# Performance work log

Hardware: AMD Instinct MI355X
Metric: run time of the kernel (lower is better)

## Reference

```python
import jax, jax.numpy as jnp
import numpy as np

N = 8192
HIDDEN = 1024
PROJ = 128
T = 0.07
LN_EPS = 1e-12


def _neg_indices(n):
    # Static [n, n-2] index matrix: for row i, all j except j==i and the
    # paired sample j == (i + n//2) % n. Computed with numpy (n is static).
    half = n // 2
    idx = np.arange(n)
    mask = np.ones((n, n), dtype=bool)
    mask[idx, idx] = False
    mask[idx, (idx + half) % n] = False
    return np.nonzero(mask)[1].reshape(n, n - 2)


def setup_inputs() -> dict:
    key = jax.random.key(0)
    ks = jax.random.split(key, 3)
    scale = 1.0 / np.sqrt(HIDDEN)
    return {
        "x": jax.random.normal(ks[0], (N, HIDDEN), dtype=jnp.float32),
        "dense_w": jax.random.normal(ks[1], (HIDDEN, HIDDEN), dtype=jnp.float32) * scale,
        "dense_b": jnp.zeros((HIDDEN,), dtype=jnp.float32),
        "ln_gamma": jnp.ones((HIDDEN,), dtype=jnp.float32),
        "ln_beta": jnp.zeros((HIDDEN,), dtype=jnp.float32),
        "dec_w": jax.random.normal(ks[2], (HIDDEN, PROJ), dtype=jnp.float32) * scale,
        "dec_b": jnp.zeros((PROJ,), dtype=jnp.float32),
    }


def reference(x, dense_w, dense_b, ln_gamma, ln_beta, dec_w, dec_b):
    # dense -> gelu (exact, erf-based as in BERT) -> layernorm -> decoder
    h = x @ dense_w + dense_b
    h = jax.nn.gelu(h, approximate=False)
    mu = jnp.mean(h, axis=-1, keepdims=True)
    var = jnp.mean(jnp.square(h - mu), axis=-1, keepdims=True)
    h = (h - mu) * jax.lax.rsqrt(var + LN_EPS) * ln_gamma + ln_beta
    z = h @ dec_w + dec_b  # [N, 128]

    n = z.shape[0]
    half = n // 2
    # positive logit: dot(z_i, z_partner)
    l_pos = jnp.sum(z[:half] * z[half:], axis=-1)  # [N/2]
    l_pos = jnp.concatenate([l_pos, l_pos])[:, None]  # [N, 1]

    # full similarity matrix, then gather the N-2 negatives per row
    sims = z @ z.T  # [N, N]
    neg_idx = jnp.asarray(_neg_indices(n))  # static [N, N-2]
    l_neg = jnp.take_along_axis(sims, neg_idx, axis=1)  # [N, N-2]

    logits = jnp.concatenate([l_pos, l_neg], axis=1) / T  # [N, N-1]
    # CrossEntropyLoss with labels == 0
    loss = jnp.mean(jax.nn.logsumexp(logits, axis=-1) - logits[:, 0])
    return loss
```

## Files before the change

kernel.cpp:

```cpp
#include <hip/hip_runtime.h>
#include <math.h>
#include <stdint.h>

#define NN 8192
#define HID 1024
#define PROJ 128

constexpr float INV_T = 1.0f / 0.07f;
constexpr float LN_EPS = 1e-12f;
constexpr float CC = 14.285714285714286f * 1.4426950408889634f;

typedef __bf16 bf16x8 __attribute__((ext_vector_type(8)));
typedef float f32x4 __attribute__((ext_vector_type(4)));

#define EXP2(x) __builtin_amdgcn_exp2f(x)

#define GLD16(g, l)                                                     \
  __builtin_amdgcn_global_load_lds(                                     \
      (const __attribute__((address_space(1))) uint32_t*)(g),           \
      (__attribute__((address_space(3))) uint32_t*)(l), 16, 0, 0)

__device__ __forceinline__ uint16_t f2bf(float f) {
  union { float f; uint32_t u; } c; c.f = f;
  uint32_t r = (c.u + 0x7FFFu + ((c.u >> 16) & 1u)) >> 16;
  return (uint16_t)r;
}
__device__ __forceinline__ float bf2f(uint16_t u) {
  union { uint32_t u; float f; } c; c.u = ((uint32_t)u) << 16;
  return c.f;
}

__device__ __forceinline__ float gelu_f(float v) {
  float w = v * v;
  float u = v * fmaf(w, 0.0356774081f, 0.7978845608f);
  float e = EXP2(u * -2.8853900818f);
  return v * __builtin_amdgcn_rcpf(1.0f + e);
}

__global__ __launch_bounds__(256) void k_conv(const float* __restrict__ in,
                                              uint16_t* __restrict__ out,
                                              float* __restrict__ sums,
                                              float* __restrict__ c_e) {
  const int b = blockIdx.x, t = threadIdx.x;
  if (b < 64) sums[b * 256 + t] = 0.f;
  else if (b == 64) c_e[t] = 0.f;
  int i = (b * 256 + t) * 4;
  float4 v = *(const float4*)(in + i);
  ushort4 o;
  o.x = f2bf(v.x); o.y = f2bf(v.y); o.z = f2bf(v.z); o.w = f2bf(v.w);
  *(ushort4*)(out + i) = o;
}

__global__ __launch_bounds__(256) void k_t1(const float* __restrict__ in,
                                            uint16_t* __restrict__ out,
                                            int R, int C) {
  __shared__ uint16_t t[32][33];
  const int cb = blockIdx.x * 32, rb = blockIdx.y * 32;
  const int tr = threadIdx.x >> 3, tc4 = (threadIdx.x & 7) * 4;
  float4 v = *(const float4*)(in + (size_t)(rb + tr) * C + cb + tc4);
  t[tc4 + 0][tr] = f2bf(v.x);
  t[tc4 + 1][tr] = f2bf(v.y);
  t[tc4 + 2][tr] = f2bf(v.z);
  t[tc4 + 3][tr] = f2bf(v.w);
  __syncthreads();
  const int oc = threadIdx.x >> 3, or4 = (threadIdx.x & 7) * 4;
  ushort4 o;
  o.x = t[oc][or4 + 0]; o.y = t[oc][or4 + 1];
  o.z = t[oc][or4 + 2]; o.w = t[oc][or4 + 3];
  *(ushort4*)(out + (size_t)(cb + oc) * R + rb + or4) = o;
}

__global__ __launch_bounds__(256) void k_t2(const float* __restrict__ in,
                                            const float* __restrict__ gamma,
                                            const float* __restrict__ beta,
                                            uint16_t* __restrict__ out,
                                            float* __restrict__ c_e) {
  __shared__ float tg[32][33];
  __shared__ float tb[32][33];
  const int cb = blockIdx.x * 32, rb = blockIdx.y * 32;
  const int tr = threadIdx.x >> 3, tc4 = (threadIdx.x & 7) * 4;
  const float g = gamma[rb + tr], be = beta[rb + tr];
  float4 v = *(const float4*)(in + (size_t)(rb + tr) * PROJ + cb + tc4);
  tg[tc4 + 0][tr] = g * v.x;  tb[tc4 + 0][tr] = be * v.x;
  tg[tc4 + 1][tr] = g * v.y;  tb[tc4 + 1][tr] = be * v.y;
  tg[tc4 + 2][tr] = g * v.z;  tb[tc4 + 2][tr] = be * v.z;
  tg[tc4 + 3][tr] = g * v.w;  tb[tc4 + 3][tr] = be * v.w;
  __syncthreads();
  const int oc = threadIdx.x >> 3, or4 = (threadIdx.x & 7) * 4;
  ushort4 o;
  o.x = f2bf(tg[oc][or4 + 0]); o.y = f2bf(tg[oc][or4 + 1]);
  o.z = f2bf(tg[oc][or4 + 2]); o.w = f2bf(tg[oc][or4 + 3]);
  *(ushort4*)(out + (size_t)(cb + oc) * HID + rb + or4) = o;
  if (threadIdx.x < 32) {
    float sc = 0.f, se = 0.f;
#pragma unroll
    for (int d = 0; d < 32; ++d) { sc += tg[threadIdx.x][d]; se += tb[threadIdx.x][d]; }
    atomicAdd(c_e + cb + threadIdx.x, sc);
    atomicAdd(c_e + 128 + cb + threadIdx.x, se);
  }
}

__global__ __launch_bounds__(256) void k_gemm1(
    const uint16_t* __restrict__ Ab, const uint16_t* __restrict__ Bt,
    const float* __restrict__ bias, uint16_t* __restrict__ Hout,
    float* __restrict__ sums) {
  __shared__ __align__(16) uint16_t As[2 * 64 * 32];
  __shared__ __align__(16) uint16_t Bs[2 * 128 * 32];
  const int tid = threadIdx.x;
  const int bn = blockIdx.x * 128, bm = blockIdx.y * 64;
  const int wave = tid >> 6, lane = tid & 63;
  const int wx = wave & 1, wy = wave >> 1;
  const int col = lane & 15, quad = lane >> 4;
  f32x4 acc[2][4] = {};
  const char* Abase = (const char*)Ab;
  const char* Bbase = (const char*)Bt;
  for (int k0 = 0; k0 < HID; k0 += 64) {
    __syncthreads();
#pragma unroll
    for (int l = 0; l < 2; ++l) {
      int off = tid * 16 + l * 4096;
      int h = off >> 12, row = (off >> 6) & 63, inner = off & 63;
      GLD16(Abase + ((size_t)(bm + row) * HID + k0 + h * 32) * 2 + inner,
            (char*)As + off);
    }
#pragma unroll
    for (int l = 0; l < 4; ++l) {
      int off = tid * 16 + l * 4096;
      int h = off >> 13, row = (off >> 6) & 127, inner = off & 63;
      GLD16(Bbase + ((size_t)(bn + row) * HID + k0 + h * 32) * 2 + inner,
            (char*)Bs + off);
    }
    __syncthreads();
#pragma unroll
    for (int h = 0; h < 2; ++h) {
      bf16x8 a[2], b[4];
#pragma unroll
      for (int mt = 0; mt < 2; ++mt)
        a[mt] = *(const bf16x8*)&As[h * 2048 +
                                    (wy * 32 + mt * 16 + col) * 32 + quad * 8];
#pragma unroll
      for (int nt = 0; nt < 4; ++nt)
        b[nt] = *(const bf16x8*)&Bs[h * 4096 +
                                    (wx * 64 + nt * 16 + col) * 32 + quad * 8];
#pragma unroll
      for (int mt = 0; mt < 2; ++mt)
#pragma unroll
        for (int nt = 0; nt < 4; ++nt)
          acc[mt][nt] = __builtin_amdgcn_mfma_f32_16x16x32_bf16(
              a[mt], b[nt], acc[mt][nt], 0, 0, 0);
    }
  }
  float rsum[2][4] = {}, rsq[2][4] = {};
#pragma unroll
  for (int nt = 0; nt < 4; ++nt) {
    int gj = bn + wx * 64 + nt * 16 + col;
    float bv = bias[gj];
#pragma unroll
    for (int mt = 0; mt < 2; ++mt)
#pragma unroll
      for (int r = 0; r < 4; ++r) {
        int gi = bm + wy * 32 + mt * 16 + quad * 4 + r;
        float gl = gelu_f(acc[mt][nt][r] + bv);
        Hout[(size_t)gi * HID + gj] = f2bf(gl);
        rsum[mt][r] += gl;
        rsq[mt][r] = fmaf(gl, gl, rsq[mt][r]);
      }
  }
#pragma unroll
  for (int mt = 0; mt < 2; ++mt)
#pragma unroll
    for (int r = 0; r < 4; ++r) {
      float s1 = rsum[mt][r], s2 = rsq[mt][r];
#pragma unroll
      for (int off = 1; off < 16; off <<= 1) {
        s1 += __shfl_xor(s1, off, 64);
        s2 += __shfl_xor(s2, off, 64);
      }
      if (col == 0) {
        int gi = bm + wy * 32 + mt * 16 + quad * 4 + r;
        atomicAdd(&sums[gi], s1);
        atomicAdd(&sums[NN + gi], s2);
      }
    }
}

__global__ __launch_bounds__(256) void k_gemm2(
    const uint16_t* __restrict__ Hb, const uint16_t* __restrict__ Wt2,
    const float* __restrict__ bd, const float* __restrict__ sums,
    const float* __restrict__ c_e, uint16_t* __restrict__ Z) {
  __shared__ __align__(16) uint16_t As2[32 * 32];
  __shared__ __align__(16) uint16_t Bs2[128 * 32];
  __shared__ float muS[32], rS[32];
  const int tid = threadIdx.x;
  const int bm = blockIdx.x * 32;
  const int wave = tid >> 6, lane = tid & 63;
  const int wx = wave & 1, wy = wave >> 1;
  const int col = lane & 15, quad = lane >> 4;
  if (tid < 32) {
    float s = sums[bm + tid], q = sums[NN + bm + tid];
    float mu = s * (1.0f / HID);
    float var = q * (1.0f / HID) - mu * mu;
    muS[tid] = mu;
    rS[tid] = rsqrtf(var + LN_EPS);
  }
  f32x4 acc[4] = {};
  const char* Abase = (const char*)Hb;
  const char* Bbase = (const char*)Wt2;
  for (int k0 = 0; k0 < HID; k0 += 32) {
    __syncthreads();
    if (tid < 128) {
      int off = tid * 16;
      int row = off >> 6, inner = off & 63;
      GLD16(Abase + ((size_t)(bm + row) * HID + k0) * 2 + inner,
            (char*)As2 + off);
    }
#pragma unroll
    for (int l = 0; l < 2; ++l) {
      int off = tid * 16 + l * 4096;
      int row = off >> 6, inner = off & 63;
      GLD16(Bbase + ((size_t)row * HID + k0) * 2 + inner, (char*)Bs2 + off);
    }
    __syncthreads();
    bf16x8 a = *(const bf16x8*)&As2[(wy * 16 + col) * 32 + quad * 8];
#pragma unroll
    for (int nt = 0; nt < 4; ++nt) {
      bf16x8 b = *(const bf16x8*)&Bs2[(wx * 64 + nt * 16 + col) * 32 + quad * 8];
      acc[nt] = __builtin_amdgcn_mfma_f32_16x16x32_bf16(a, b, acc[nt], 0, 0, 0);
    }
  }
#pragma unroll
  for (int nt = 0; nt < 4; ++nt) {
    int gj = wx * 64 + nt * 16 + col;
    float ck = c_e[gj], ek = c_e[128 + gj] + bd[gj];
#pragma unroll
    for (int r = 0; r < 4; ++r) {
      int li = wy * 16 + quad * 4 + r;
      float mu = muS[li], rr = rS[li];
      float z = fmaf(rr, acc[nt][r], fmaf(-rr * mu, ck, ek));
      Z[(size_t)(bm + li) * PROJ + gj] = f2bf(z);
    }
  }
}

__device__ __forceinline__ void lse4(float& m, float& s, float v0, float v1,
                                     float v2, float v3) {
  float lm = fmaxf(fmaxf(v0, v1), fmaxf(v2, v3));
  float mn = fmaxf(m, lm);
  float tn = mn * CC;
  float rs = EXP2(fmaf(m, CC, -tn));
  float e = EXP2(fmaf(v0, CC, -tn)) + EXP2(fmaf(v1, CC, -tn)) +
            EXP2(fmaf(v2, CC, -tn)) + EXP2(fmaf(v3, CC, -tn));
  s = fmaf(s, rs, e);
  m = mn;
}

__global__ __launch_bounds__(256) void k_sim(const uint16_t* __restrict__ Z,
                                             float* __restrict__ m_part,
                                             float* __restrict__ s_part,
                                             float* __restrict__ pos_arr) {
  __shared__ __align__(16) uint16_t Bsh[2][64 * 128];
  const int tid = threadIdx.x;
  const int wave = tid >> 6, lane = tid & 63;
  const int col = lane & 15, quad = lane >> 4;
  const int wrow0 = blockIdx.x * 128 + wave * 32;
  const int chunk = blockIdx.y;
  const char* Zb = (const char*)Z;

  bf16x8 afr[2][4];
#pragma unroll
  for (int mt = 0; mt < 2; ++mt)
#pragma unroll
    for (int kc = 0; kc < 4; ++kc)
      afr[mt][kc] = *(const bf16x8*)(Z +
          (size_t)(wrow0 + mt * 16 + col) * PROJ + kc * 32 + quad * 8);

  float ms[8], ss[8];
#pragma unroll
  for (int i = 0; i < 8; ++i) { ms[i] = -INFINITY; ss[i] = 0.f; }

  const int diag_t = wrow0 & ~63;
  const int pos_t = ((wrow0 + NN / 2) & (NN - 1)) & ~63;
  const int jbase = chunk * 512;

#define STAGE(t, bufv)                                                      \
  {                                                                         \
    const int j0s = jbase + (t) * 64;                                       \
    _Pragma("unroll") for (int l = 0; l < 4; ++l) {                         \
      int off = tid * 16 + l * 4096;                                        \
      int row = off >> 8;                                                   \
      int p = (off >> 4) & 15;                                              \
      GLD16(Zb + (size_t)(j0s + row) * 256 + ((p ^ (row & 7)) << 4),        \
            (char*)&Bsh[bufv][0] + off);                                    \
    }                                                                       \
  }

  STAGE(0, 0);
  for (int t = 0; t < 8; ++t) {
    const int buf = t & 1;
    __syncthreads();
    if (t < 7) STAGE(t + 1, buf ^ 1);
    const int jt = jbase + t * 64;
    f32x4 acc[2][4] = {};
#pragma unroll
    for (int kc = 0; kc < 4; ++kc) {
      bf16x8 b[4];
#pragma unroll
      for (int nt = 0; nt < 4; ++nt) {
        int r = nt * 16 + col;
        b[nt] = *(const bf16x8*)&Bsh[buf][r * 128 +
                                         (((kc * 4 + quad) ^ (col & 7)) << 3)];
      }
#pragma unroll
      for (int mt = 0; mt < 2; ++mt)
#pragma unroll
        for (int nt = 0; nt < 4; ++nt)
          acc[mt][nt] = __builtin_amdgcn_mfma_f32_16x16x32_bf16(
              afr[mt][kc], b[nt], acc[mt][nt], 0, 0, 0);
    }
    if (jt != diag_t && jt != pos_t) {
#pragma unroll
      for (int mt = 0; mt < 2; ++mt)
#pragma unroll
        for (int r = 0; r < 4; ++r)
          lse4(ms[mt * 4 + r], ss[mt * 4 + r], acc[mt][0][r], acc[mt][1][r],
               acc[mt][2][r], acc[mt][3][r]);
    } else {
      const bool isd = (jt == diag_t);
#pragma unroll
      for (int mt = 0; mt < 2; ++mt)
#pragma unroll
        for (int r = 0; r < 4; ++r) {
          int gi = wrow0 + mt * 16 + quad * 4 + r;
          int partner = (gi + NN / 2) & (NN - 1);
          float v[4];
#pragma unroll
          for (int nt = 0; nt < 4; ++nt) {
            int gj = jt + nt * 16 + col;
            float d = acc[mt][nt][r];
            if (!isd && gj == partner) pos_arr[gi] = d;
            v[nt] = (isd && gj == gi) ? -INFINITY : d;
          }
          lse4(ms[mt * 4 + r], ss[mt * 4 + r], v[0], v[1], v[2], v[3]);
        }
    }
  }
#undef STAGE
#pragma unroll
  for (int ri = 0; ri < 8; ++ri) {
#pragma unroll
    for (int off = 1; off < 16; off <<= 1) {
      float om = __shfl_xor(ms[ri], off, 64);
      float os = __shfl_xor(ss[ri], off, 64);
      float mn = fmaxf(ms[ri], om);
      float tn = mn * CC;
      ss[ri] = fmaf(ss[ri], EXP2(fmaf(ms[ri], CC, -tn)),
                    os * EXP2(fmaf(om, CC, -tn)));
      ms[ri] = mn;
    }
  }
  if (col == 0) {
#pragma unroll
    for (int ri = 0; ri < 8; ++ri) {
      int gi = wrow0 + (ri >> 2) * 16 + quad * 4 + (ri & 3);
      m_part[(size_t)chunk * NN + gi] = ms[ri];
      s_part[(size_t)chunk * NN + gi] = ss[ri];
    }
  }
}

__global__ __launch_bounds__(256) void k_combine(
    const float* __restrict__ m_part, const float* __restrict__ s_part,
    const float* __restrict__ pos_arr, float* __restrict__ row_loss) {
  const int i = blockIdx.x * 256 + threadIdx.x;
  float M = -INFINITY;
#pragma unroll
  for (int p = 0; p < 16; ++p) M = fmaxf(M, m_part[(size_t)p * NN + i]);
  float S = 0.f;
  float t = M * CC;
#pragma unroll
  for (int p = 0; p < 16; ++p)
    S += s_part[(size_t)p * NN + i] * EXP2(fmaf(m_part[(size_t)p * NN + i], CC, -t));
  row_loss[i] = (M - pos_arr[i]) * INV_T + logf(S);
}

__global__ __launch_bounds__(256) void k_final(
    const float* __restrict__ row_loss, float* __restrict__ out) {
  const int tid = threadIdx.x;
  float s = 0.f;
#pragma unroll
  for (int l = 0; l < 32; ++l) s += row_loss[tid + l * 256];
#pragma unroll
  for (int off = 32; off > 0; off >>= 1) s += __shfl_down(s, off);
  __shared__ float red[4];
  const int wave = tid >> 6, lane = tid & 63;
  if (lane == 0) red[wave] = s;
  __syncthreads();
  if (tid == 0) out[0] = (red[0] + red[1] + red[2] + red[3]) * (1.0f / NN);
}

extern "C" void kernel_launch(void* const* d_in, const int* in_sizes, int n_in,
                              void* d_out, int out_size, void* d_ws,
                              size_t ws_size, hipStream_t stream) {
  const float* x       = (const float*)d_in[0];
  const float* dense_w = (const float*)d_in[1];
  const float* dense_b = (const float*)d_in[2];
  const float* ln_g    = (const float*)d_in[3];
  const float* ln_b    = (const float*)d_in[4];
  const float* dec_w   = (const float*)d_in[5];
  const float* dec_b   = (const float*)d_in[6];
  float* out = (float*)d_out;
  char* ws = (char*)d_ws;
  uint16_t* xb      = (uint16_t*)(ws);
  uint16_t* wt      = (uint16_t*)(ws + 16777216);
  uint16_t* h       = (uint16_t*)(ws + 18874368);
  uint16_t* z       = (uint16_t*)(ws);
  float*    m_part  = (float*)(ws + 16777216);
  float*    s_part  = (float*)(ws + 17301504);
  uint16_t* wt2     = (uint16_t*)(ws + 35651584);
  float*    sums    = (float*)(ws + 35913728);
  float*    c_e     = (float*)(ws + 35979264);
  float*    pos_arr = (float*)(ws + 35980288);
  float*    row_loss= (float*)(ws + 36013056);

  k_conv<<<dim3(NN * HID / 1024), 256, 0, stream>>>(x, xb, sums, c_e);
  k_t1<<<dim3(32, 32), 256, 0, stream>>>(dense_w, wt, HID, HID);
  k_t2<<<dim3(PROJ / 32, HID / 32), 256, 0, stream>>>(dec_w, ln_g, ln_b, wt2,
                                                      c_e);
  k_gemm1<<<dim3(8, 128), 256, 0, stream>>>(xb, wt, dense_b, h, sums);
  k_gemm2<<<dim3(NN / 32), 256, 0, stream>>>(h, wt2, dec_b, sums, c_e, z);
  k_sim<<<dim3(NN / 128, 16), 256, 0, stream>>>(z, m_part, s_part, pos_arr);
  k_combine<<<dim3(NN / 256), 256, 0, stream>>>(m_part, s_part, pos_arr,
                                                row_loss);
  k_final<<<dim3(1), 256, 0, stream>>>(row_loss, out);
}
```

Baseline: 178.9 us.

## Double-buffer GEMM K-loops and fuse prep and final-reduce kernels

Merges the bf16 conversion and two weight transposes into one prep launch, replacing column-sum atomics with per-block partials reduced in gemm2. Both GEMMs get double-buffered LDS with prefetch of the next K slice after a single barrier per iteration. The final mean reduction is folded into the combine kernel using an atomic counter for last-block completion. This cuts launch count and hides global-load latency, at the cost of doubled LDS usage and a reliance on atomic ordering.

```diff
diff --git a/kernel.cpp b/kernel.cpp
--- a/kernel.cpp
+++ b/kernel.cpp
@@ -24,10 +24,6 @@
   union { float f; uint32_t u; } c; c.f = f;
   uint32_t r = (c.u + 0x7FFFu + ((c.u >> 16) & 1u)) >> 16;
   return (uint16_t)r;
-}
-__device__ __forceinline__ float bf2f(uint16_t u) {
-  union { uint32_t u; float f; } c; c.u = ((uint32_t)u) << 16;
-  return c.f;
 }
 
 __device__ __forceinline__ float gelu_f(float v) {
@@ -37,66 +33,64 @@
   return v * __builtin_amdgcn_rcpf(1.0f + e);
 }
 
-__global__ __launch_bounds__(256) void k_conv(const float* __restrict__ in,
-                                              uint16_t* __restrict__ out,
-                                              float* __restrict__ sums,
-                                              float* __restrict__ c_e) {
+__global__ __launch_bounds__(256) void k_prep(
+    const float* __restrict__ x, uint16_t* __restrict__ xb,
+    const float* __restrict__ dw, uint16_t* __restrict__ wt,
+    const float* __restrict__ decw, const float* __restrict__ gamma,
+    const float* __restrict__ beta, uint16_t* __restrict__ wt2,
+    float* __restrict__ sums, float* __restrict__ c_part,
+    float* __restrict__ accum) {
+  __shared__ __align__(16) char sm[8448];
   const int b = blockIdx.x, t = threadIdx.x;
-  if (b < 64) sums[b * 256 + t] = 0.f;
-  else if (b == 64) c_e[t] = 0.f;
-  int i = (b * 256 + t) * 4;
-  float4 v = *(const float4*)(in + i);
-  ushort4 o;
-  o.x = f2bf(v.x); o.y = f2bf(v.y); o.z = f2bf(v.z); o.w = f2bf(v.w);
-  *(ushort4*)(out + i) = o;
-}
-
-__global__ __launch_bounds__(256) void k_t1(const float* __restrict__ in,
-                                            uint16_t* __restrict__ out,
-                                            int R, int C) {
-  __shared__ uint16_t t[32][33];
-  const int cb = blockIdx.x * 32, rb = blockIdx.y * 32;
-  const int tr = threadIdx.x >> 3, tc4 = (threadIdx.x & 7) * 4;
-  float4 v = *(const float4*)(in + (size_t)(rb + tr) * C + cb + tc4);
-  t[tc4 + 0][tr] = f2bf(v.x);
-  t[tc4 + 1][tr] = f2bf(v.y);
-  t[tc4 + 2][tr] = f2bf(v.z);
-  t[tc4 + 3][tr] = f2bf(v.w);
-  __syncthreads();
-  const int oc = threadIdx.x >> 3, or4 = (threadIdx.x & 7) * 4;
-  ushort4 o;
-  o.x = t[oc][or4 + 0]; o.y = t[oc][or4 + 1];
-  o.z = t[oc][or4 + 2]; o.w = t[oc][or4 + 3];
-  *(ushort4*)(out + (size_t)(cb + oc) * R + rb + or4) = o;
-}
-
-__global__ __launch_bounds__(256) void k_t2(const float* __restrict__ in,
-                                            const float* __restrict__ gamma,
-                                            const float* __restrict__ beta,
-                                            uint16_t* __restrict__ out,
-                                            float* __restrict__ c_e) {
-  __shared__ float tg[32][33];
-  __shared__ float tb[32][33];
-  const int cb = blockIdx.x * 32, rb = blockIdx.y * 32;
-  const int tr = threadIdx.x >> 3, tc4 = (threadIdx.x & 7) * 4;
-  const float g = gamma[rb + tr], be = beta[rb + tr];
-  float4 v = *(const float4*)(in + (size_t)(rb + tr) * PROJ + cb + tc4);
-  tg[tc4 + 0][tr] = g * v.x;  tb[tc4 + 0][tr] = be * v.x;
-  tg[tc4 + 1][tr] = g * v.y;  tb[tc4 + 1][tr] = be * v.y;
-  tg[tc4 + 2][tr] = g * v.z;  tb[tc4 + 2][tr] = be * v.z;
-  tg[tc4 + 3][tr] = g * v.w;  tb[tc4 + 3][tr] = be * v.w;
-  __syncthreads();
-  const int oc = threadIdx.x >> 3, or4 = (threadIdx.x & 7) * 4;
-  ushort4 o;
-  o.x = f2bf(tg[oc][or4 + 0]); o.y = f2bf(tg[oc][or4 + 1]);
-  o.z = f2bf(tg[oc][or4 + 2]); o.w = f2bf(tg[oc][or4 + 3]);
-  *(ushort4*)(out + (size_t)(cb + oc) * HID + rb + or4) = o;
-  if (threadIdx.x < 32) {
-    float sc = 0.f, se = 0.f;
-#pragma unroll
-    for (int d = 0; d < 32; ++d) { sc += tg[threadIdx.x][d]; se += tb[threadIdx.x][d]; }
-    atomicAdd(c_e + cb + threadIdx.x, sc);
-    atomicAdd(c_e + 128 + cb + threadIdx.x, se);
+  if (b < 8192) {
+    if (b < 64) sums[b * 256 + t] = 0.f;
+    else if (b == 64 && t < 2) accum[t] = 0.f;
+    int i = (b * 256 + t) * 4;
+    float4 v = *(const float4*)(x + i);
+    ushort4 o;
+    o.x = f2bf(v.x); o.y = f2bf(v.y); o.z = f2bf(v.z); o.w = f2bf(v.w);
+    *(ushort4*)(xb + i) = o;
+  } else if (b < 9216) {
+    uint16_t (*tt)[33] = (uint16_t(*)[33])sm;
+    const int lb = b - 8192;
+    const int cb = (lb & 31) * 32, rb = (lb >> 5) * 32;
+    const int tr = t >> 3, tc4 = (t & 7) * 4;
+    float4 v = *(const float4*)(dw + (size_t)(rb + tr) * HID + cb + tc4);
+    tt[tc4 + 0][tr] = f2bf(v.x);
+    tt[tc4 + 1][tr] = f2bf(v.y);
+    tt[tc4 + 2][tr] = f2bf(v.z);
+    tt[tc4 + 3][tr] = f2bf(v.w);
+    __syncthreads();
+    const int oc = t >> 3, or4 = (t & 7) * 4;
+    ushort4 o;
+    o.x = tt[oc][or4 + 0]; o.y = tt[oc][or4 + 1];
+    o.z = tt[oc][or4 + 2]; o.w = tt[oc][or4 + 3];
+    *(ushort4*)(wt + (size_t)(cb + oc) * HID + rb + or4) = o;
+  } else {
+    float (*tg)[33] = (float(*)[33])sm;
+    float (*tb)[33] = (float(*)[33])(sm + 4224);
+    const int lb = b - 9216;
+    const int cb = (lb & 3) * 32, rb = (lb >> 2) * 32;
+    const int tr = t >> 3, tc4 = (t & 7) * 4;
+    const float g = gamma[rb + tr], be = beta[rb + tr];
+    float4 v = *(const float4*)(decw + (size_t)(rb + tr) * PROJ + cb + tc4);
+    tg[tc4 + 0][tr] = g * v.x;  tb[tc4 + 0][tr] = be * v.x;
+    tg[tc4 + 1][tr] = g * v.y;  tb[tc4 + 1][tr] = be * v.y;
+    tg[tc4 + 2][tr] = g * v.z;  tb[tc4 + 2][tr] = be * v.z;
+    tg[tc4 + 3][tr] = g * v.w;  tb[tc4 + 3][tr] = be * v.w;
+    __syncthreads();
+    const int oc = t >> 3, or4 = (t & 7) * 4;
+    ushort4 o;
+    o.x = f2bf(tg[oc][or4 + 0]); o.y = f2bf(tg[oc][or4 + 1]);
+    o.z = f2bf(tg[oc][or4 + 2]); o.w = f2bf(tg[oc][or4 + 3]);
+    *(ushort4*)(wt2 + (size_t)(cb + oc) * HID + rb + or4) = o;
+    if (t < 32) {
+      float sc = 0.f, se = 0.f;
+#pragma unroll
+      for (int d = 0; d < 32; ++d) { sc += tg[t][d]; se += tb[t][d]; }
+      c_part[(rb >> 5) * 128 + cb + t] = sc;
+      c_part[4096 + (rb >> 5) * 128 + cb + t] = se;
+    }
   }
 }
 
@@ -104,8 +98,8 @@
     const uint16_t* __restrict__ Ab, const uint16_t* __restrict__ Bt,
     const float* __restrict__ bias, uint16_t* __restrict__ Hout,
     float* __restrict__ sums) {
-  __shared__ __align__(16) uint16_t As[2 * 64 * 32];
-  __shared__ __align__(16) uint16_t Bs[2 * 128 * 32];
+  __shared__ __align__(16) uint16_t As[2][2 * 64 * 32];
+  __shared__ __align__(16) uint16_t Bs[2][2 * 128 * 32];
   const int tid = threadIdx.x;
   const int bn = blockIdx.x * 128, bm = blockIdx.y * 64;
   const int wave = tid >> 6, lane = tid & 63;
@@ -114,34 +108,41 @@
   f32x4 acc[2][4] = {};
   const char* Abase = (const char*)Ab;
   const char* Bbase = (const char*)Bt;
-  for (int k0 = 0; k0 < HID; k0 += 64) {
+
+#define G1STAGE(k0v, bufv)                                                   \
+  {                                                                          \
+    _Pragma("unroll") for (int l = 0; l < 2; ++l) {                          \
+      int off = tid * 16 + l * 4096;                                         \
+      int hh = off >> 12, row = (off >> 6) & 63, inner = off & 63;           \
+      GLD16(Abase + ((size_t)(bm + row) * HID + (k0v) + hh * 32) * 2 + inner,\
+            (char*)&As[bufv][0] + off);                                      \
+    }                                                                        \
+    _Pragma("unroll") for (int l = 0; l < 4; ++l) {                          \
+      int off = tid * 16 + l * 4096;                                         \
+      int hh = off >> 13, row = (off >> 6) & 127, inner = off & 63;          \
+      GLD16(Bbase + ((size_t)(bn + row) * HID + (k0v) + hh * 32) * 2 + inner,\
+            (char*)&Bs[bufv][0] + off);                                      \
+    }                                                                        \
+  }
+
+  G1STAGE(0, 0);
+  for (int it = 0; it < 16; ++it) {
+    const int buf = it & 1;
     __syncthreads();
-#pragma unroll
-    for (int l = 0; l < 2; ++l) {
-      int off = tid * 16 + l * 4096;
-      int h = off >> 12, row = (off >> 6) & 63, inner = off & 63;
-      GLD16(Abase + ((size_t)(bm + row) * HID + k0 + h * 32) * 2 + inner,
-            (char*)As + off);
-    }
-#pragma unroll
-    for (int l = 0; l < 4; ++l) {
-      int off = tid * 16 + l * 4096;
-      int h = off >> 13, row = (off >> 6) & 127, inner = off & 63;
-      GLD16(Bbase + ((size_t)(bn + row) * HID + k0 + h * 32) * 2 + inner,
-            (char*)Bs + off);
-    }
-    __syncthreads();
+    if (it < 15) G1STAGE((it + 1) * 64, buf ^ 1);
 #pragma unroll
     for (int h = 0; h < 2; ++h) {
       bf16x8 a[2], b[4];
 #pragma unroll
       for (int mt = 0; mt < 2; ++mt)
-        a[mt] = *(const bf16x8*)&As[h * 2048 +
-                                    (wy * 32 + mt * 16 + col) * 32 + quad * 8];
+        a[mt] = *(const bf16x8*)&As[buf][h * 2048 +
+                                        (wy * 32 + mt * 16 + col) * 32 +
+                                        quad * 8];
 #pragma unroll
       for (int nt = 0; nt < 4; ++nt)
-        b[nt] = *(const bf16x8*)&Bs[h * 4096 +
-                                    (wx * 64 + nt * 16 + col) * 32 + quad * 8];
+        b[nt] = *(const bf16x8*)&Bs[buf][h * 4096 +
+                                         (wx * 64 + nt * 16 + col) * 32 +
+                                         quad * 8];
 #pragma unroll
       for (int mt = 0; mt < 2; ++mt)
 #pragma unroll
@@ -150,6 +151,7 @@
               a[mt], b[nt], acc[mt][nt], 0, 0, 0);
     }
   }
+#undef G1STAGE
   float rsum[2][4] = {}, rsq[2][4] = {};
 #pragma unroll
   for (int nt = 0; nt < 4; ++nt) {
@@ -187,15 +189,35 @@
 __global__ __launch_bounds__(256) void k_gemm2(
     const uint16_t* __restrict__ Hb, const uint16_t* __restrict__ Wt2,
     const float* __restrict__ bd, const float* __restrict__ sums,
-    const float* __restrict__ c_e, uint16_t* __restrict__ Z) {
-  __shared__ __align__(16) uint16_t As2[32 * 32];
-  __shared__ __align__(16) uint16_t Bs2[128 * 32];
-  __shared__ float muS[32], rS[32];
+    const float* __restrict__ c_part, uint16_t* __restrict__ Z) {
+  __shared__ __align__(16) uint16_t As2[2][32 * 32];
+  __shared__ __align__(16) uint16_t Bs2[2][128 * 32];
+  __shared__ float muS[32], rS[32], ckS[128], ekS[128];
   const int tid = threadIdx.x;
   const int bm = blockIdx.x * 32;
   const int wave = tid >> 6, lane = tid & 63;
   const int wx = wave & 1, wy = wave >> 1;
   const int col = lane & 15, quad = lane >> 4;
+  const char* Abase = (const char*)Hb;
+  const char* Bbase = (const char*)Wt2;
+
+#define G2STAGE(k0v, bufv)                                                   \
+  {                                                                          \
+    if (tid < 128) {                                                         \
+      int off = tid * 16;                                                    \
+      int row = off >> 6, inner = off & 63;                                  \
+      GLD16(Abase + ((size_t)(bm + row) * HID + (k0v)) * 2 + inner,          \
+            (char*)&As2[bufv][0] + off);                                     \
+    }                                                                        \
+    _Pragma("unroll") for (int l = 0; l < 2; ++l) {                          \
+      int off = tid * 16 + l * 4096;                                         \
+      int row = off >> 6, inner = off & 63;                                  \
+      GLD16(Bbase + ((size_t)row * HID + (k0v)) * 2 + inner,                 \
+            (char*)&Bs2[bufv][0] + off);                                     \
+    }                                                                        \
+  }
+
+  G2STAGE(0, 0);
   if (tid < 32) {
     float s = sums[bm + tid], q = sums[NN + bm + tid];
     float mu = s * (1.0f / HID);
@@ -203,35 +225,34 @@
     muS[tid] = mu;
     rS[tid] = rsqrtf(var + LN_EPS);
   }
+  if (tid < 128) {
+    float sc = 0.f, se = 0.f;
+#pragma unroll 4
+    for (int p = 0; p < 32; ++p) {
+      sc += c_part[p * 128 + tid];
+      se += c_part[4096 + p * 128 + tid];
+    }
+    ckS[tid] = sc;
+    ekS[tid] = se + bd[tid];
+  }
   f32x4 acc[4] = {};
-  const char* Abase = (const char*)Hb;
-  const char* Bbase = (const char*)Wt2;
-  for (int k0 = 0; k0 < HID; k0 += 32) {
+  for (int it = 0; it < 32; ++it) {
+    const int buf = it & 1;
     __syncthreads();
-    if (tid < 128) {
-      int off = tid * 16;
-      int row = off >> 6, inner = off & 63;
-      GLD16(Abase + ((size_t)(bm + row) * HID + k0) * 2 + inner,
-            (char*)As2 + off);
-    }
-#pragma unroll
-    for (int l = 0; l < 2; ++l) {
-      int off = tid * 16 + l * 4096;
-      int row = off >> 6, inner = off & 63;
-      GLD16(Bbase + ((size_t)row * HID + k0) * 2 + inner, (char*)Bs2 + off);
-    }
-    __syncthreads();
-    bf16x8 a = *(const bf16x8*)&As2[(wy * 16 + col) * 32 + quad * 8];
+    if (it < 31) G2STAGE((it + 1) * 32, buf ^ 1);
+    bf16x8 a = *(const bf16x8*)&As2[buf][(wy * 16 + col) * 32 + quad * 8];
 #pragma unroll
     for (int nt = 0; nt < 4; ++nt) {
-      bf16x8 b = *(const bf16x8*)&Bs2[(wx * 64 + nt * 16 + col) * 32 + quad * 8];
+      bf16x8 b =
+          *(const bf16x8*)&Bs2[buf][(wx * 64 + nt * 16 + col) * 32 + quad * 8];
       acc[nt] = __builtin_amdgcn_mfma_f32_16x16x32_bf16(a, b, acc[nt], 0, 0, 0);
     }
   }
+#undef G2STAGE
 #pragma unroll
   for (int nt = 0; nt < 4; ++nt) {
     int gj = wx * 64 + nt * 16 + col;
-    float ck = c_e[gj], ek = c_e[128 + gj] + bd[gj];
+    float ck = ckS[gj], ek = ekS[gj];
 #pragma unroll
     for (int r = 0; r < 4; ++r) {
       int li = wy * 16 + quad * 4 + r;
@@ -308,7 +329,7 @@
       for (int nt = 0; nt < 4; ++nt) {
         int r = nt * 16 + col;
         b[nt] = *(const bf16x8*)&Bsh[buf][r * 128 +
-                                         (((kc * 4 + quad) ^ (col & 7)) << 3)];
+                                          (((kc * 4 + quad) ^ (col & 7)) << 3)];
       }
 #pragma unroll
       for (int mt = 0; mt < 2; ++mt)
@@ -370,8 +391,10 @@
 
 __global__ __launch_bounds__(256) void k_combine(
     const float* __restrict__ m_part, const float* __restrict__ s_part,
-    const float* __restrict__ pos_arr, float* __restrict__ row_loss) {
-  const int i = blockIdx.x * 256 + threadIdx.x;
+    const float* __restrict__ pos_arr, float* __restrict__ accum,
+    float* __restrict__ out) {
+  const int tid = threadIdx.x;
+  const int i = blockIdx.x * 256 + tid;
   float M = -INFINITY;
 #pragma unroll
   for (int p = 0; p < 16; ++p) M = fmaxf(M, m_part[(size_t)p * NN + i]);
@@ -379,23 +402,25 @@
   float t = M * CC;
 #pragma unroll
   for (int p = 0; p < 16; ++p)
-    S += s_part[(size_t)p * NN + i] * EXP2(fmaf(m_part[(size_t)p * NN + i], CC, -t));
-  row_loss[i] = (M - pos_arr[i]) * INV_T + logf(S);
-}
-
-__global__ __launch_bounds__(256) void k_final(
-    const float* __restrict__ row_loss, float* __restrict__ out) {
-  const int tid = threadIdx.x;
-  float s = 0.f;
-#pragma unroll
-  for (int l = 0; l < 32; ++l) s += row_loss[tid + l * 256];
-#pragma unroll
-  for (int off = 32; off > 0; off >>= 1) s += __shfl_down(s, off);
+    S += s_part[(size_t)p * NN + i] *
+         EXP2(fmaf(m_part[(size_t)p * NN + i], CC, -t));
+  float rl = (M - pos_arr[i]) * INV_T + logf(S);
+#pragma unroll
+  for (int off = 32; off > 0; off >>= 1) rl += __shfl_down(rl, off);
   __shared__ float red[4];
   const int wave = tid >> 6, lane = tid & 63;
-  if (lane == 0) red[wave] = s;
+  if (lane == 0) red[wave] = rl;
   __syncthreads();
-  if (tid == 0) out[0] = (red[0] + red[1] + red[2] + red[3]) * (1.0f / NN);
+  if (tid == 0) {
+    float part = red[0] + red[1] + red[2] + red[3];
+    atomicAdd(&accum[0], part);
+    __threadfence();
+    int old = atomicAdd((int*)&accum[1], 1);
+    if (old == 31) {
+      float tot = atomicAdd(&accum[0], 0.0f);
+      out[0] = tot * (1.0f / NN);
+    }
+  }
 }
 
 extern "C" void kernel_launch(void* const* d_in, const int* in_sizes, int n_in,
@@ -418,18 +443,15 @@
   float*    s_part  = (float*)(ws + 17301504);
   uint16_t* wt2     = (uint16_t*)(ws + 35651584);
   float*    sums    = (float*)(ws + 35913728);
-  float*    c_e     = (float*)(ws + 35979264);
-  float*    pos_arr = (float*)(ws + 35980288);
-  float*    row_loss= (float*)(ws + 36013056);
-
-  k_conv<<<dim3(NN * HID / 1024), 256, 0, stream>>>(x, xb, sums, c_e);
-  k_t1<<<dim3(32, 32), 256, 0, stream>>>(dense_w, wt, HID, HID);
-  k_t2<<<dim3(PROJ / 32, HID / 32), 256, 0, stream>>>(dec_w, ln_g, ln_b, wt2,
-                                                      c_e);
+  float*    c_part  = (float*)(ws + 35979264);
+  float*    pos_arr = (float*)(ws + 36012032);
+  float*    accum   = (float*)(ws + 36044800);
+
+  k_prep<<<dim3(9344), 256, 0, stream>>>(x, xb, dense_w, wt, dec_w, ln_g,
+                                         ln_b, wt2, sums, c_part, accum);
   k_gemm1<<<dim3(8, 128), 256, 0, stream>>>(xb, wt, dense_b, h, sums);
-  k_gemm2<<<dim3(NN / 32), 256, 0, stream>>>(h, wt2, dec_b, sums, c_e, z);
+  k_gemm2<<<dim3(NN / 32), 256, 0, stream>>>(h, wt2, dec_b, sums, c_part, z);
   k_sim<<<dim3(NN / 128, 16), 256, 0, stream>>>(z, m_part, s_part, pos_arr);
   k_combine<<<dim3(NN / 256), 256, 0, stream>>>(m_part, s_part, pos_arr,
-                                                row_loss);
-  k_final<<<dim3(1), 256, 0, stream>>>(row_loss, out);
-}
+                                                accum, out);
+}
```

Measured after the change: 183.8 us. 1.03x slower.
